# Kernel tuning notes

Measured on AMD Instinct MI355X. Metric: run time of the kernel, lower is better.

## Reference

```python
import jax, jax.numpy as jnp
import numpy as np

N_HEAD = 50000
N_TAIL = 50000
E = 1600000
IN_F = 256
OUT_F = 32
NHEAD = 4
EDGE_F = 64
N_ETYPES = 5
NEG_SLOPE = 0.2


def setup_inputs() -> dict:
    key = jax.random.key(0)
    ks = jax.random.split(key, 10)
    return {
        "head_feature": jax.random.normal(ks[0], (N_HEAD, IN_F), jnp.float32),
        "tail_feature": jax.random.normal(ks[1], (N_TAIL, IN_F), jnp.float32),
        "W": jax.random.normal(ks[2], (IN_F, OUT_F * NHEAD), jnp.float32) * 0.05,
        "W_e": jax.random.normal(ks[3], (EDGE_F, EDGE_F * NHEAD), jnp.float32) * 0.05,
        "edge_emb": jax.random.normal(ks[4], (N_ETYPES, EDGE_F), jnp.float32) * 0.1,
        "a_l": jax.random.normal(ks[5], (1, NHEAD, OUT_F), jnp.float32) * 0.1,
        "a_r": jax.random.normal(ks[6], (1, NHEAD, OUT_F), jnp.float32) * 0.1,
        "a_e": jax.random.normal(ks[7], (1, NHEAD, EDGE_F), jnp.float32) * 0.1,
        "edge_list": jax.random.randint(ks[8], (2, E), 0, N_HEAD, jnp.int64),
        "tmp_edge": jax.random.randint(ks[9], (E,), 0, N_ETYPES, jnp.int64),
    }


def reference(head_feature, tail_feature, W, W_e, edge_emb, a_l, a_r, a_e, edge_list, tmp_edge):
    n_head_nodes = head_feature.shape[0]
    nhead, out_dim = a_l.shape[1], a_l.shape[2]
    edge_feats = a_e.shape[2]

    # dense projections (dropout in eval mode = identity)
    h_head = (head_feature @ W).reshape(-1, nhead, out_dim)   # [Nh, H, D]
    h_tail = (tail_feature @ W).reshape(-1, nhead, out_dim)   # [Nt, H, D]
    e = (edge_emb @ W_e).reshape(-1, nhead, edge_feats)       # [T,  H, De]

    head_ind = edge_list[0]
    tail_ind = edge_list[1]

    # per-edge attention logits [E, H]
    h_e = (a_e * e).sum(-1)[tmp_edge]
    h_l = (a_l * h_head).sum(-1)[head_ind]
    h_r = (a_r * h_tail).sum(-1)[tail_ind]
    att = jax.nn.leaky_relu(h_l + h_r + h_e, negative_slope=NEG_SLOPE)

    # sparse softmax over dim=1 (per head-node row), per head
    m = jax.ops.segment_max(att, head_ind, num_segments=n_head_nodes)
    m = jnp.where(jnp.isfinite(m), m, jnp.zeros_like(m))  # empty rows
    ex = jnp.exp(att - m[head_ind])
    denom = jax.ops.segment_sum(ex, head_ind, num_segments=n_head_nodes)
    alpha = ex / denom[head_ind]                              # [E, H]

    # sparse-mm aggregation: out[i] = sum_e alpha_e * h_tail[tail_e]
    msg = alpha[..., None] * h_tail[tail_ind]                 # [E, H, D]
    out = jax.ops.segment_sum(msg, head_ind, num_segments=n_head_nodes)
    out = out.reshape(n_head_nodes, nhead * out_dim)
    out = jax.nn.elu(out)
    return out, alpha
```

## Files before the change

kernel.cpp:

```cpp
#include <hip/hip_runtime.h>
#include <hip/hip_bf16.h>
#include <string.h>

#define NNODE 50000
#define NEDGE 1600000
#define INF   256
#define NH    4
#define EF    64
#define NET   5

#define NBUCK 782
#define BCAP  2560
#define EPB   2048
#define PBLK  782
#define BKS   784
#define RDB   1563

typedef unsigned short u16t;
typedef __attribute__((ext_vector_type(8))) short short8;
typedef __attribute__((ext_vector_type(4))) float f32x4;

__device__ __forceinline__ float b2f(u16t u) {
    union { unsigned int i; float f; } v; v.i = ((unsigned int)u) << 16; return v.f;
}
__device__ __forceinline__ u16t f2b(float f) {
    __hip_bfloat16 h = __float2bfloat16(f);
    u16t u; memcpy(&u, &h, 2); return u;
}

__global__ void k_pre(const float* __restrict__ W, const float* __restrict__ We,
                      const float* __restrict__ emb, const float* __restrict__ al,
                      const float* __restrict__ ar, const float* __restrict__ ae,
                      const int* __restrict__ el, const int* __restrict__ ety,
                      float* __restrict__ wl, float* __restrict__ wr,
                      float* __restrict__ he, int* __restrict__ flag,
                      u16t* __restrict__ Wfrag) {
    int b = blockIdx.x;
    int tid = threadIdx.x;
    if (b == 0) {
        if (tid < 128) {
            int w = tid >> 6, lane = tid & 63;
            const int* p = (w == 0) ? el : ety;
            int x = p[2 * lane + 1];
            unsigned long long bal = __ballot(x != 0);
            if (lane == 0) flag[w] = (bal == 0ULL) ? 1 : 0;
        }
    } else if (b == 1) {
        __shared__ float wes[EF * NH];
        {
            int k = tid;
            for (int h = 0; h < NH; h++) {
                float accl = 0.f, accr = 0.f;
                for (int d = 0; d < 32; d++) {
                    float w = W[k * 128 + h * 32 + d];
                    accl += w * al[h * 32 + d];
                    accr += w * ar[h * 32 + d];
                }
                wl[k * NH + h] = accl;
                wr[k * NH + h] = accr;
            }
        }
        if (tid < EF) {
            int k = tid;
            for (int h = 0; h < NH; h++) {
                float s = 0.f;
                for (int d = 0; d < EF; d++)
                    s += We[k * (NH * EF) + h * EF + d] * ae[h * EF + d];
                wes[k * NH + h] = s;
            }
        }
        __syncthreads();
        if (tid < NET * NH) {
            int t = tid / NH, h = tid % NH;
            float s = 0.f;
            for (int k = 0; k < EF; k++)
                s += emb[t * EF + k] * wes[k * NH + h];
            he[tid] = s;
        }
    } else {
        int idx = (b - 2) * 256 + tid;
        int j    = idx & 7;
        int lane = (idx >> 3) & 63;
        int ks   = (idx >> 9) & 7;
        int tile = idx >> 12;
        int n = tile * 16 + (lane & 15);
        int k = ks * 32 + (lane >> 4) * 8 + j;
        Wfrag[idx] = f2b(W[k * 128 + n]);
    }
}

__global__ void k_fuseA(const float* __restrict__ head,
                        const float* __restrict__ wl,
                        const int* __restrict__ el, const int* __restrict__ ety,
                        const int* __restrict__ flag,
                        int* __restrict__ hist2d, int* __restrict__ loff2d,
                        unsigned int* __restrict__ bucketbuf,
                        float* __restrict__ hl) {
    __shared__ unsigned int srec[EPB];
    __shared__ int hist[BKS];
    __shared__ int loff[BKS];
    __shared__ int psum[256];
    int b = blockIdx.x;
    int tid = threadIdx.x;
    if (b < PBLK) {
        int base = b * EPB;
        int wf = flag[0], wt = flag[1];
        for (int i = tid; i < BKS; i += 256) hist[i] = 0;
        __syncthreads();
        unsigned int rec[8];
        unsigned int br[8];
#pragma unroll
        for (int i = 0; i < 8; i++) {
            int e = base + i * 256 + tid;
            br[i] = 0xffffffffu;
            rec[i] = 0;
            if (e < NEDGE) {
                int hi = wf ? el[2 * (long long)e]           : el[e];
                int ti = wf ? el[2 * ((long long)NEDGE + e)] : el[NEDGE + e];
                int ty = wt ? ety[2 * (long long)e]          : ety[e];
                int bk = hi >> 6;
                int r = atomicAdd(&hist[bk], 1);
                rec[i] = (unsigned)ti | ((unsigned)(hi & 63) << 16) | ((unsigned)ty << 22);
                br[i]  = (unsigned)bk | ((unsigned)r << 16);
            }
        }
        __syncthreads();
        int s4[4]; int tsum = 0;
        if (tid < 196) {
#pragma unroll
            for (int j = 0; j < 4; j++) { s4[j] = hist[4 * tid + j]; tsum += s4[j]; }
        }
        psum[tid] = (tid < 196) ? tsum : 0;
        __syncthreads();
        for (int off = 1; off < 256; off <<= 1) {
            int v = (tid >= off) ? psum[tid - off] : 0;
            __syncthreads();
            psum[tid] += v;
            __syncthreads();
        }
        if (tid < 196) {
            int run = tid ? psum[tid - 1] : 0;
#pragma unroll
            for (int j = 0; j < 4; j++) {
                int bk = 4 * tid + j;
                loff[bk] = run;
                hist2d[b * BKS + bk] = s4[j];
                loff2d[b * BKS + bk] = run;
                run += s4[j];
            }
        }
        __syncthreads();
#pragma unroll
        for (int i = 0; i < 8; i++) {
            if (br[i] != 0xffffffffu) {
                int bk = br[i] & 0xffff;
                int r  = br[i] >> 16;
                srec[loff[bk] + r] = rec[i];
            }
        }
        __syncthreads();
        int tot = psum[255];
        for (int i = tid; i < tot; i += 256)
            bucketbuf[(size_t)b * EPB + i] = srec[i];
    } else {
        int bb = b - PBLK;
        int rowbase = bb * 32;
        int wave = tid >> 6;
        int g = (tid >> 4) & 3;
        int l = tid & 15;
        const float4* wv4 = (const float4*)wl;
        float4 acc[2];
#pragma unroll
        for (int rr = 0; rr < 2; rr++) {
            acc[rr].x = 0.f; acc[rr].y = 0.f; acc[rr].z = 0.f; acc[rr].w = 0.f;
            int row = rowbase + rr * 16 + wave * 4 + g;
            if (row < NNODE) {
                const float* xp = head + (size_t)row * INF + l * 4;
#pragma unroll
                for (int c = 0; c < 4; c++) {
                    float4 xv = *(const float4*)(xp + c * 64);
                    float xs[4] = {xv.x, xv.y, xv.z, xv.w};
#pragma unroll
                    for (int j = 0; j < 4; j++) {
                        float4 wvv = wv4[c * 64 + l * 4 + j];
                        acc[rr].x += xs[j] * wvv.x;
                        acc[rr].y += xs[j] * wvv.y;
                        acc[rr].z += xs[j] * wvv.z;
                        acc[rr].w += xs[j] * wvv.w;
                    }
                }
            }
        }
#pragma unroll
        for (int rr = 0; rr < 2; rr++) {
#pragma unroll
            for (int off = 8; off > 0; off >>= 1) {
                acc[rr].x += __shfl_xor(acc[rr].x, off);
                acc[rr].y += __shfl_xor(acc[rr].y, off);
                acc[rr].z += __shfl_xor(acc[rr].z, off);
                acc[rr].w += __shfl_xor(acc[rr].w, off);
            }
            int row = rowbase + rr * 16 + wave * 4 + g;
            if (l == 0 && row < NNODE) ((float4*)hl)[row] = acc[rr];
        }
    }
}

__global__ void k_bsum(const int* __restrict__ hist2d, int* __restrict__ cursor) {
    __shared__ int red[256];
    int bk = blockIdx.x;
    int tid = threadIdx.x;
    int s = 0;
    for (int sb = tid; sb < PBLK; sb += 256) s += hist2d[sb * BKS + bk];
    red[tid] = s;
    __syncthreads();
    for (int off = 128; off > 0; off >>= 1) {
        if (tid < off) red[tid] += red[tid + off];
        __syncthreads();
    }
    if (tid == 0) cursor[bk] = red[0];
}

__global__ void k_bscan(const int* __restrict__ cursor, int* __restrict__ bstart,
                        int* __restrict__ row_start) {
    __shared__ int psum[256];
    int tid = threadIdx.x;
    int s4[4]; int tsum = 0;
    if (tid < 196) {
#pragma unroll
        for (int j = 0; j < 4; j++) {
            int bk = 4 * tid + j;
            s4[j] = (bk < NBUCK) ? cursor[bk] : 0;
            tsum += s4[j];
        }
    }
    psum[tid] = (tid < 196) ? tsum : 0;
    __syncthreads();
    for (int off = 1; off < 256; off <<= 1) {
        int v = (tid >= off) ? psum[tid - off] : 0;
        __syncthreads();
        psum[tid] += v;
        __syncthreads();
    }
    if (tid < 196) {
        int run = tid ? psum[tid - 1] : 0;
#pragma unroll
        for (int j = 0; j < 4; j++) {
            int bk = 4 * tid + j;
            if (bk < NBUCK) bstart[bk] = run;
            run += s4[j];
        }
    }
    if (tid == 255) {
        bstart[NBUCK] = psum[255];
        row_start[NNODE] = psum[255];
    }
}

__global__ void k_fuseB(const float* __restrict__ X, const u16t* __restrict__ Wfrag,
                        const float* __restrict__ ar,
                        u16t* __restrict__ H, float* __restrict__ hr,
                        const unsigned int* __restrict__ bucketbuf,
                        const int* __restrict__ hist2d, const int* __restrict__ loff2d,
                        const int* __restrict__ bstart,
                        unsigned int* __restrict__ cpack, int* __restrict__ row_start) {
    __shared__ __attribute__((aligned(16))) u16t alds[16 * 264];
    __shared__ unsigned int lrec[BCAP];
    __shared__ unsigned int lord[BCAP];
    __shared__ int psum[256];
    __shared__ int cnt[64];
    __shared__ int sc[64];
    int b = blockIdx.x;
    int tid = threadIdx.x;
    if (b < 3125) {
        int rowbase = b * 16;
        for (int i = tid; i < 1024; i += 256) {
            int row = i >> 6;
            int kc = (i & 63) * 4;
            float4 v = *(const float4*)(X + (size_t)(rowbase + row) * INF + kc);
            u16t* d = alds + row * 264 + kc;
            d[0] = f2b(v.x); d[1] = f2b(v.y); d[2] = f2b(v.z); d[3] = f2b(v.w);
        }
        __syncthreads();
        int wave = tid >> 6, lane = tid & 63;
        int m = lane & 15, quad = lane >> 4;
        int t0 = wave * 2, t1 = t0 + 1;
        f32x4 acc0 = {0.f, 0.f, 0.f, 0.f};
        f32x4 acc1 = {0.f, 0.f, 0.f, 0.f};
#pragma unroll
        for (int ks = 0; ks < 8; ks++) {
            short8 a  = *(const short8*)(alds + m * 264 + ks * 32 + quad * 8);
            short8 b0 = *(const short8*)(Wfrag + (((t0 * 8 + ks) * 64 + lane) << 3));
            short8 b1 = *(const short8*)(Wfrag + (((t1 * 8 + ks) * 64 + lane) << 3));
            acc0 = __builtin_amdgcn_mfma_f32_16x16x32_bf16(a, b0, acc0, 0, 0, 0);
            acc1 = __builtin_amdgcn_mfma_f32_16x16x32_bf16(a, b1, acc1, 0, 0, 0);
        }
        u16t* Hp = H + (size_t)rowbase * 128;
#pragma unroll
        for (int r = 0; r < 4; r++) {
            int row = quad * 4 + r;
            Hp[(size_t)row * 128 + t0 * 16 + m] = f2b(acc0[r]);
            Hp[(size_t)row * 128 + t1 * 16 + m] = f2b(acc1[r]);
        }
        float arm0 = ar[wave * 32 + m];
        float arm1 = ar[wave * 32 + 16 + m];
#pragma unroll
        for (int r = 0; r < 4; r++) {
            float p = arm0 * acc0[r] + arm1 * acc1[r];
#pragma unroll
            for (int off = 8; off > 0; off >>= 1) p += __shfl_xor(p, off);
            if (m == 0) hr[(rowbase + quad * 4 + r) * 4 + wave] = p;
        }
    } else {
        int q = b - 3125;
        int bs = bstart[q];
        int c4[4], o4[4]; int tsum = 0;
        if (tid < 196) {
#pragma unroll
            for (int j = 0; j < 4; j++) {
                int sb = 4 * tid + j;
                c4[j] = 0; o4[j] = 0;
                if (sb < PBLK) {
                    c4[j] = hist2d[sb * BKS + q];
                    o4[j] = loff2d[sb * BKS + q];
                }
                tsum += c4[j];
            }
        }
        psum[tid] = (tid < 196) ? tsum : 0;
        __syncthreads();
        for (int off = 1; off < 256; off <<= 1) {
            int v = (tid >= off) ? psum[tid - off] : 0;
            __syncthreads();
            psum[tid] += v;
            __syncthreads();
        }
        if (tid < 196) {
            int run = tid ? psum[tid - 1] : 0;
#pragma unroll
            for (int j = 0; j < 4; j++) {
                int sb = 4 * tid + j;
                for (int k = 0; k < c4[j]; k++) {
                    int d = run + k;
                    if (d < BCAP)
                        lrec[d] = bucketbuf[(size_t)sb * EPB + o4[j] + k];
                }
                run += c4[j];
            }
        }
        if (tid < 64) cnt[tid] = 0;
        __syncthreads();
        int nrec = psum[255];
        if (nrec > BCAP) nrec = BCAP;
        unsigned int myr[10];
        int k2 = 0;
        for (int i = tid; i < nrec; i += 256) {
            int n = (lrec[i] >> 16) & 63;
            myr[k2++] = atomicAdd(&cnt[n], 1);
        }
        __syncthreads();
        if (tid < 64) sc[tid] = cnt[tid];
        __syncthreads();
        for (int off = 1; off < 64; off <<= 1) {
            int v = (tid >= off && tid < 64) ? sc[tid - off] : 0;
            __syncthreads();
            if (tid < 64) sc[tid] += v;
            __syncthreads();
        }
        k2 = 0;
        for (int i = tid; i < nrec; i += 256) {
            unsigned int rc = lrec[i];
            int n  = (rc >> 16) & 63;
            int ti = rc & 0xffff;
            int ty = rc >> 22;
            int pos = (sc[n] - cnt[n]) + (int)myr[k2++];
            lord[pos] = ((unsigned)ty << 18) | (unsigned)ti;
        }
        __syncthreads();
        for (int i = tid; i < nrec; i += 256)
            cpack[bs + i] = lord[i];
        if (tid < 64) {
            int node = q * 64 + tid;
            if (node < NNODE) row_start[node] = bs + (sc[tid] - cnt[tid]);
        }
    }
}

__global__ void k_agg(const int* __restrict__ rs, const unsigned int* __restrict__ cpack,
                      const float* __restrict__ hl, const float* __restrict__ hr,
                      const float* __restrict__ heg, const u16t* __restrict__ ht,
                      float* __restrict__ den, float2* __restrict__ out) {
    __shared__ float hes[NET * NH];
    int tid = threadIdx.x;
    if (tid < NET * NH) hes[tid] = heg[tid];
    __syncthreads();
    int wave = tid >> 6, lane = tid & 63;
    int node = blockIdx.x * 4 + wave;
    int start = rs[node], end = rs[node + 1];
    unsigned h = (unsigned)(lane >> 4);
    unsigned lane2 = (unsigned)(lane << 1);
    float hlv = hl[(unsigned)node * 4u + h];
    const float* hesh = hes + h;
    float a0 = 0.f, a1 = 0.f, s = 0.f;
    int j = start;
    for (; j + 4 <= end; j += 4) {
        unsigned c0 = cpack[j], c1 = cpack[j + 1], c2 = cpack[j + 2], c3 = cpack[j + 3];
        unsigned t0 = c0 & 0xffffu, t1 = c1 & 0xffffu;
        unsigned t2 = c2 & 0xffffu, t3 = c3 & 0xffffu;
        float r0 = hr[(t0 << 2) + h], r1 = hr[(t1 << 2) + h];
        float r2 = hr[(t2 << 2) + h], r3 = hr[(t3 << 2) + h];
        unsigned v0 = *(const unsigned*)(ht + ((t0 << 7) + lane2));
        unsigned v1 = *(const unsigned*)(ht + ((t1 << 7) + lane2));
        unsigned v2 = *(const unsigned*)(ht + ((t2 << 7) + lane2));
        unsigned v3 = *(const unsigned*)(ht + ((t3 << 7) + lane2));
        float x0 = hlv + r0 + hesh[c0 >> 16];
        float x1 = hlv + r1 + hesh[c1 >> 16];
        float x2 = hlv + r2 + hesh[c2 >> 16];
        float x3 = hlv + r3 + hesh[c3 >> 16];
        x0 = fmaxf(x0, 0.2f * x0);
        x1 = fmaxf(x1, 0.2f * x1);
        x2 = fmaxf(x2, 0.2f * x2);
        x3 = fmaxf(x3, 0.2f * x3);
        float e0 = __expf(x0), e1 = __expf(x1), e2 = __expf(x2), e3 = __expf(x3);
        union { unsigned u; float f; } w0, w1;
        w0.u = v0 << 16;          w1.u = v0 & 0xffff0000u;
        a0 += e0 * w0.f;          a1 += e0 * w1.f;
        w0.u = v1 << 16;          w1.u = v1 & 0xffff0000u;
        a0 += e1 * w0.f;          a1 += e1 * w1.f;
        w0.u = v2 << 16;          w1.u = v2 & 0xffff0000u;
        a0 += e2 * w0.f;          a1 += e2 * w1.f;
        w0.u = v3 << 16;          w1.u = v3 & 0xffff0000u;
        a0 += e3 * w0.f;          a1 += e3 * w1.f;
        s  += e0 + e1 + e2 + e3;
    }
    for (; j < end; j++) {
        unsigned c = cpack[j];
        unsigned ti = c & 0xffffu;
        float att = hlv + hr[(ti << 2) + h] + hesh[c >> 16];
        att = fmaxf(att, 0.2f * att);
        float exv = __expf(att);
        unsigned hv = *(const unsigned*)(ht + ((ti << 7) + lane2));
        union { unsigned u; float f; } w0, w1;
        w0.u = hv << 16;  w1.u = hv & 0xffff0000u;
        a0 += exv * w0.f;
        a1 += exv * w1.f;
        s  += exv;
    }
    if ((lane & 15) == 0) den[(unsigned)node * 4u + h] = s;
    float o0 = 0.f, o1 = 0.f;
    if (s > 0.f) { o0 = a0 / s; o1 = a1 / s; }
    o0 = o0 > 0.f ? o0 : expm1f(o0);
    o1 = o1 > 0.f ? o1 : expm1f(o1);
    float2 ov = {o0, o1};
    out[(size_t)node * 64 + lane] = ov;
}

__global__ void k_alpha(const int* __restrict__ el, const int* __restrict__ ety,
                        const int* __restrict__ flag,
                        const float* __restrict__ hl, const float* __restrict__ hr,
                        const float* __restrict__ heg, const float* __restrict__ den,
                        float* __restrict__ alpha) {
    __shared__ float hes[NET * NH];
    int tid = threadIdx.x;
    if (tid < NET * NH) hes[tid] = heg[tid];
    __syncthreads();
    int wf = flag[0], wt = flag[1];
    int e = blockIdx.x * 256 + tid;
    int hi = wf ? el[2 * (long long)e]           : el[e];
    int ti = wf ? el[2 * ((long long)NEDGE + e)] : el[NEDGE + e];
    int ty = wt ? ety[2 * (long long)e]          : ety[e];
    float4 l = ((const float4*)hl)[hi];
    float4 r = ((const float4*)hr)[ti];
    float4 d = ((const float4*)den)[hi];
    float v0 = l.x + r.x + hes[ty * 4 + 0];
    float v1 = l.y + r.y + hes[ty * 4 + 1];
    float v2 = l.z + r.z + hes[ty * 4 + 2];
    float v3 = l.w + r.w + hes[ty * 4 + 3];
    v0 = v0 > 0.f ? v0 : 0.2f * v0;
    v1 = v1 > 0.f ? v1 : 0.2f * v1;
    v2 = v2 > 0.f ? v2 : 0.2f * v2;
    v3 = v3 > 0.f ? v3 : 0.2f * v3;
    float4 o;
    o.x = d.x > 0.f ? __expf(v0) / d.x : 0.f;
    o.y = d.y > 0.f ? __expf(v1) / d.y : 0.f;
    o.z = d.z > 0.f ? __expf(v2) / d.z : 0.f;
    o.w = d.w > 0.f ? __expf(v3) / d.w : 0.f;
    ((float4*)alpha)[e] = o;
}

extern "C" void kernel_launch(void* const* d_in, const int* in_sizes, int n_in,
                              void* d_out, int out_size, void* d_ws, size_t ws_size,
                              hipStream_t stream) {
    const float* head = (const float*)d_in[0];
    const float* tail = (const float*)d_in[1];
    const float* W    = (const float*)d_in[2];
    const float* We   = (const float*)d_in[3];
    const float* emb  = (const float*)d_in[4];
    const float* al   = (const float*)d_in[5];
    const float* ar   = (const float*)d_in[6];
    const float* ae   = (const float*)d_in[7];
    const int*   el   = (const int*)d_in[8];
    const int*   ety  = (const int*)d_in[9];

    float* ws = (float*)d_ws;
    float* hl       = ws;
    float* hr       = ws + 200000;
    float* wl       = ws + 400000;
    float* wr       = ws + 401024;
    float* heg      = ws + 402048;
    int*   flag     = (int*)(ws + 402080);
    int*   bstart   = (int*)(ws + 402096);
    int*   cursor   = (int*)(ws + 402880);
    float* den      = ws + 403664;
    int*   row_start= (int*)(ws + 603664);
    u16t*  Wfrag    = (u16t*)(ws + 653668);

    float* outp   = (float*)d_out;
    float* alphap = (float*)d_out + 6400000;
    u16t*         htail = (u16t*)alphap;
    unsigned int* cpack = (unsigned int*)(alphap + 3200000);
    unsigned int* bucketbuf = (unsigned int*)outp;
    int* hist2d = (int*)outp + 1601536;
    int* loff2d = hist2d + 613088;

    k_pre<<<130, 256, 0, stream>>>(W, We, emb, al, ar, ae, el, ety,
                                   wl, wr, heg, flag, Wfrag);
    k_fuseA<<<PBLK + RDB, 256, 0, stream>>>(head, wl, el, ety, flag,
                                            hist2d, loff2d, bucketbuf, hl);
    k_bsum<<<NBUCK, 256, 0, stream>>>(hist2d, cursor);
    k_bscan<<<1, 256, 0, stream>>>(cursor, bstart, row_start);
    k_fuseB<<<3125 + NBUCK, 256, 0, stream>>>(tail, Wfrag, ar, htail, hr, bucketbuf,
                                              hist2d, loff2d, bstart, cpack, row_start);
    k_agg<<<NNODE / 4, 256, 0, stream>>>(row_start, cpack, hl, hr, heg, htail,
                                         den, (float2*)outp);
    k_alpha<<<NEDGE / 256, 256, 0, stream>>>(el, ety, flag, hl, hr, heg, den, alphap);
}
```

Baseline: 326.0 us.

## Drop global bucket prefix scan; use fixed-capacity bucket slots with per-node row ends

Removes the bucket-sum and single-block scan kernels by giving each bucket a fixed slot of BCAP entries in the packed edge array, and stores an explicit row_end per node so the aggregation kernel no longer needs contiguous row offsets. This cuts two kernel launches and a serial single-block dependency from the chain. In exchange it uses a sparser cpack layout, needs extra scratch for row_end in the output region, and relies on no bucket exceeding BCAP edges.

```diff
diff --git a/kernel.cpp b/kernel.cpp
--- a/kernel.cpp
+++ b/kernel.cpp
@@ -206,64 +206,13 @@
     }
 }
 
-__global__ void k_bsum(const int* __restrict__ hist2d, int* __restrict__ cursor) {
-    __shared__ int red[256];
-    int bk = blockIdx.x;
-    int tid = threadIdx.x;
-    int s = 0;
-    for (int sb = tid; sb < PBLK; sb += 256) s += hist2d[sb * BKS + bk];
-    red[tid] = s;
-    __syncthreads();
-    for (int off = 128; off > 0; off >>= 1) {
-        if (tid < off) red[tid] += red[tid + off];
-        __syncthreads();
-    }
-    if (tid == 0) cursor[bk] = red[0];
-}
-
-__global__ void k_bscan(const int* __restrict__ cursor, int* __restrict__ bstart,
-                        int* __restrict__ row_start) {
-    __shared__ int psum[256];
-    int tid = threadIdx.x;
-    int s4[4]; int tsum = 0;
-    if (tid < 196) {
-#pragma unroll
-        for (int j = 0; j < 4; j++) {
-            int bk = 4 * tid + j;
-            s4[j] = (bk < NBUCK) ? cursor[bk] : 0;
-            tsum += s4[j];
-        }
-    }
-    psum[tid] = (tid < 196) ? tsum : 0;
-    __syncthreads();
-    for (int off = 1; off < 256; off <<= 1) {
-        int v = (tid >= off) ? psum[tid - off] : 0;
-        __syncthreads();
-        psum[tid] += v;
-        __syncthreads();
-    }
-    if (tid < 196) {
-        int run = tid ? psum[tid - 1] : 0;
-#pragma unroll
-        for (int j = 0; j < 4; j++) {
-            int bk = 4 * tid + j;
-            if (bk < NBUCK) bstart[bk] = run;
-            run += s4[j];
-        }
-    }
-    if (tid == 255) {
-        bstart[NBUCK] = psum[255];
-        row_start[NNODE] = psum[255];
-    }
-}
-
 __global__ void k_fuseB(const float* __restrict__ X, const u16t* __restrict__ Wfrag,
                         const float* __restrict__ ar,
                         u16t* __restrict__ H, float* __restrict__ hr,
                         const unsigned int* __restrict__ bucketbuf,
                         const int* __restrict__ hist2d, const int* __restrict__ loff2d,
-                        const int* __restrict__ bstart,
-                        unsigned int* __restrict__ cpack, int* __restrict__ row_start) {
+                        unsigned int* __restrict__ cpack,
+                        int* __restrict__ row_start, int* __restrict__ row_end) {
     __shared__ __attribute__((aligned(16))) u16t alds[16 * 264];
     __shared__ unsigned int lrec[BCAP];
     __shared__ unsigned int lord[BCAP];
@@ -313,7 +262,7 @@
         }
     } else {
         int q = b - 3125;
-        int bs = bstart[q];
+        int bs = q * BCAP;
         int c4[4], o4[4]; int tsum = 0;
         if (tid < 196) {
 #pragma unroll
@@ -381,12 +330,16 @@
             cpack[bs + i] = lord[i];
         if (tid < 64) {
             int node = q * 64 + tid;
-            if (node < NNODE) row_start[node] = bs + (sc[tid] - cnt[tid]);
+            if (node < NNODE) {
+                row_start[node] = bs + (sc[tid] - cnt[tid]);
+                row_end[node]   = bs + sc[tid];
+            }
         }
     }
 }
 
-__global__ void k_agg(const int* __restrict__ rs, const unsigned int* __restrict__ cpack,
+__global__ void k_agg(const int* __restrict__ rs, const int* __restrict__ re,
+                      const unsigned int* __restrict__ cpack,
                       const float* __restrict__ hl, const float* __restrict__ hr,
                       const float* __restrict__ heg, const u16t* __restrict__ ht,
                       float* __restrict__ den, float2* __restrict__ out) {
@@ -396,7 +349,7 @@
     __syncthreads();
     int wave = tid >> 6, lane = tid & 63;
     int node = blockIdx.x * 4 + wave;
-    int start = rs[node], end = rs[node + 1];
+    int start = rs[node], end = re[node];
     unsigned h = (unsigned)(lane >> 4);
     unsigned lane2 = (unsigned)(lane << 1);
     float hlv = hl[(unsigned)node * 4u + h];
@@ -509,8 +462,6 @@
     float* wr       = ws + 401024;
     float* heg      = ws + 402048;
     int*   flag     = (int*)(ws + 402080);
-    int*   bstart   = (int*)(ws + 402096);
-    int*   cursor   = (int*)(ws + 402880);
     float* den      = ws + 403664;
     int*   row_start= (int*)(ws + 603664);
     u16t*  Wfrag    = (u16t*)(ws + 653668);
@@ -519,6 +470,7 @@
     float* alphap = (float*)d_out + 6400000;
     u16t*         htail = (u16t*)alphap;
     unsigned int* cpack = (unsigned int*)(alphap + 3200000);
+    int*          row_end = (int*)(alphap + 5220000);
     unsigned int* bucketbuf = (unsigned int*)outp;
     int* hist2d = (int*)outp + 1601536;
     int* loff2d = hist2d + 613088;
@@ -527,11 +479,10 @@
                                    wl, wr, heg, flag, Wfrag);
     k_fuseA<<<PBLK + RDB, 256, 0, stream>>>(head, wl, el, ety, flag,
                                             hist2d, loff2d, bucketbuf, hl);
-    k_bsum<<<NBUCK, 256, 0, stream>>>(hist2d, cursor);
-    k_bscan<<<1, 256, 0, stream>>>(cursor, bstart, row_start);
     k_fuseB<<<3125 + NBUCK, 256, 0, stream>>>(tail, Wfrag, ar, htail, hr, bucketbuf,
-                                              hist2d, loff2d, bstart, cpack, row_start);
-    k_agg<<<NNODE / 4, 256, 0, stream>>>(row_start, cpack, hl, hr, heg, htail,
-                                         den, (float2*)outp);
+                                              hist2d, loff2d, cpack,
+                                              row_start, row_end);
+    k_agg<<<NNODE / 4, 256, 0, stream>>>(row_start, row_end, cpack, hl, hr, heg,
+                                         htail, den, (float2*)outp);
     k_alpha<<<NEDGE / 256, 256, 0, stream>>>(el, ety, flag, hl, hr, heg, den, alphap);
 }
```

New measurement: 317.2 us. 1.03x faster.
